# Kernel optimization log

Hardware: AMD Instinct MI355X
Metric: run time of the kernel (lower is better)

Reference implementation:

```python
import jax, jax.numpy as jnp
import numpy as np

N = 50000       # num_nodes
R = 8           # num_relations
H = 64          # hidden_channels
C = 16          # num_classes
E = 1_600_000   # num edges (avg degree 32)
T = 8192        # number of 'author' target nodes (first T nodes after to_homogeneous)


def setup_inputs() -> dict:
    key = jax.random.key(0)
    ks = jax.random.split(key, 12)
    s = 0.02
    return {
        "edge_index": jax.random.randint(ks[0], (2, E), 0, N),
        "edge_type": jax.random.randint(ks[1], (E,), 0, R),
        "num_target": T,
        # conv1 (featureless: weight is an embedding table [R, N, H], root is [N, H])
        "weight1": jax.random.normal(ks[2], (R, N, H), jnp.float32) * s,
        "root1": jax.random.normal(ks[3], (N, H), jnp.float32) * s,
        "bias1": jnp.zeros((H,), jnp.float32),
        # conv2
        "weight2": jax.random.normal(ks[4], (R, H, H), jnp.float32) * s,
        "root2": jax.random.normal(ks[5], (H, H), jnp.float32) * s,
        "bias2": jnp.zeros((H,), jnp.float32),
        # linear head
        "lin_w": jax.random.normal(ks[6], (H, C), jnp.float32) * s,
        "lin_b": jnp.zeros((C,), jnp.float32),
    }


def reference(edge_index, edge_type, num_target, weight1, root1, bias1,
              weight2, root2, bias2, lin_w, lin_b):
    src, dst = edge_index[0], edge_index[1]
    E_ = src.shape[0]

    # PyG RGCNConv aggregates with MEAN per relation, then sums over relations.
    # Count edges per (dst node, relation) to form the per-relation mean denominator.
    seg = dst * R + edge_type                          # [E] combined (node, relation) id
    cnt = jax.ops.segment_sum(jnp.ones((E_,), jnp.float32), seg, num_segments=N * R)
    scale = (1.0 / jnp.maximum(cnt, 1.0))[seg]         # [E]

    # ---- conv1: x is None -> message = weight1[edge_type][src] (embedding lookup) ----
    m1 = weight1[edge_type, src] * scale[:, None]      # [E, H]
    h1 = jax.ops.segment_sum(m1, dst, num_segments=N)  # [N, H]
    h1 = h1 + root1 + bias1                            # root1[arange(N)] == root1
    h1 = jax.nn.elu(h1)

    # ---- conv2: message = h1[src] @ weight2[edge_type] ----
    # Precompute per-relation node transforms [R, N, H], then gather per edge.
    hr = jnp.einsum('nh,rhk->rnk', h1, weight2)        # [R, N, H]
    m2 = hr[edge_type, src] * scale[:, None]           # [E, H]
    h2 = jax.ops.segment_sum(m2, dst, num_segments=N)  # [N, H]
    h2 = h2 + h1 @ root2 + bias2
    h2 = jax.nn.elu(h2)

    # ---- linear head on the target ('author') node slice ----
    out = h2[:num_target] @ lin_w + lin_b              # [T, C]
    return out
```

## Files before the change

### kernel.cpp

```cpp
#include <hip/hip_runtime.h>

#define NNODES 50000
#define NREL   8
#define HID    64
#define NCLS   16
#define NEDGE  1600000
#define NTGT   8192
#define NBINS  (NNODES * NREL)
#define CHUNK  1024
#define NCHUNK ((NBINS + CHUNK - 1) / CHUNK)

__device__ __forceinline__ float elu1(float x) { return x > 0.f ? x : expm1f(x); }

__global__ void count_kernel(const int* __restrict__ ei, const int* __restrict__ et,
                             int* __restrict__ cnt, int* __restrict__ epos) {
  int e4 = (blockIdx.x * blockDim.x + threadIdx.x) * 4;
  if (e4 >= NEDGE) return;
  int4 d = *(const int4*)(ei + NEDGE + e4);
  int4 r = *(const int4*)(et + e4);
  int4 p;
  p.x = atomicAdd(&cnt[d.x * NREL + r.x], 1);
  p.y = atomicAdd(&cnt[d.y * NREL + r.y], 1);
  p.z = atomicAdd(&cnt[d.z * NREL + r.z], 1);
  p.w = atomicAdd(&cnt[d.w * NREL + r.w], 1);
  *(int4*)(epos + e4) = p;
}

__global__ void chunk_sum_kernel(const int* __restrict__ cnt, int* __restrict__ csum) {
  __shared__ int sw[4];
  int t = threadIdx.x, lane = t & 63, wid = t >> 6;
  int i = blockIdx.x * CHUNK + t * 4;
  int s = 0;
  if (i < NBINS) { int4 c = *(const int4*)(cnt + i); s = c.x + c.y + c.z + c.w; }
#pragma unroll
  for (int off = 32; off >= 1; off >>= 1) s += __shfl_xor(s, off);
  if (lane == 0) sw[wid] = s;
  __syncthreads();
  if (t == 0) csum[blockIdx.x] = sw[0] + sw[1] + sw[2] + sw[3];
}

__global__ void scan_csum_kernel(const int* __restrict__ csum, int* __restrict__ cbase) {
  __shared__ int sw[8];
  int t = threadIdx.x, lane = t & 63, wid = t >> 6;
  int v0 = (t < NCHUNK) ? csum[t] : 0;
  int v = v0;
#pragma unroll
  for (int off = 1; off < 64; off <<= 1) {
    int u = __shfl_up(v, off);
    if (lane >= off) v += u;
  }
  if (lane == 63) sw[wid] = v;
  __syncthreads();
  if (t == 0) {
    int run = 0;
#pragma unroll
    for (int j = 0; j < 8; ++j) { int x = sw[j]; sw[j] = run; run += x; }
  }
  __syncthreads();
  if (t < NCHUNK) cbase[t] = sw[wid] + (v - v0);
}

__global__ void scan_write_kernel(const int* __restrict__ cnt, const int* __restrict__ cbase,
                                  int* __restrict__ binptr) {
  __shared__ int sw[4];
  int t = threadIdx.x, lane = t & 63, wid = t >> 6;
  int i = blockIdx.x * CHUNK + t * 4;
  int4 c = make_int4(0, 0, 0, 0);
  if (i < NBINS) c = *(const int4*)(cnt + i);
  int p0 = c.x, p1 = p0 + c.y, p2 = p1 + c.z, s = p2 + c.w;
  int v = s;
#pragma unroll
  for (int off = 1; off < 64; off <<= 1) {
    int u = __shfl_up(v, off);
    if (lane >= off) v += u;
  }
  if (lane == 63) sw[wid] = v;
  __syncthreads();
  if (t == 0) {
    int run = 0;
#pragma unroll
    for (int j = 0; j < 4; ++j) { int x = sw[j]; sw[j] = run; run += x; }
  }
  __syncthreads();
  if (i < NBINS) {
    int excl = cbase[blockIdx.x] + sw[wid] + (v - s);
    *(int4*)(binptr + i) = make_int4(excl, excl + p0, excl + p1, excl + p2);
  }
  if (blockIdx.x == 0 && t == 0) binptr[NBINS] = NEDGE;
}

__global__ void scatter_kernel(const int* __restrict__ ei, const int* __restrict__ et,
                               const int* __restrict__ epos, const int* __restrict__ binptr,
                               int2* __restrict__ epo) {
  int e4 = (blockIdx.x * blockDim.x + threadIdx.x) * 4;
  if (e4 >= NEDGE) return;
  int4 sv = *(const int4*)(ei + e4);
  int4 dv = *(const int4*)(ei + NEDGE + e4);
  int4 rv = *(const int4*)(et + e4);
  int4 pv = *(const int4*)(epos + e4);
  int srcs[4] = {sv.x, sv.y, sv.z, sv.w};
  int dsts[4] = {dv.x, dv.y, dv.z, dv.w};
  int rels[4] = {rv.x, rv.y, rv.z, rv.w};
  int poss[4] = {pv.x, pv.y, pv.z, pv.w};
#pragma unroll
  for (int j = 0; j < 4; ++j) {
    int bin = dsts[j] * NREL + rels[j];
    int b = binptr[bin];
    int c = binptr[bin + 1] - b;
    float sc = 1.0f / (float)c;
    epo[b + poss[j]] = make_int2(rels[j] * NNODES + srcs[j], __float_as_int(sc));
  }
}

__global__ __launch_bounds__(256) void conv1_kernel(
    const int* __restrict__ binptr, const int2* __restrict__ epo,
    const float* __restrict__ w1, const float* __restrict__ root1,
    const float* __restrict__ bias1, float* __restrict__ h1) {
  int wave = blockIdx.x * 4 + (threadIdx.x >> 6);
  if (wave >= NNODES) return;
  int lane = threadIdx.x & 63;
  int b0 = binptr[wave * NREL], b8 = binptr[wave * NREL + NREL];
  float acc = 0.f;
  for (int eb = b0; eb < b8; eb += 64) {
    int mb = min(64, b8 - eb);
    int2 q = epo[eb + min(lane, mb - 1)];
    int j = 0;
    for (; j + 8 <= mb; j += 8) {
      float a[8], sc[8];
#pragma unroll
      for (int u = 0; u < 8; ++u) {
        int idx = __builtin_amdgcn_readlane(q.x, j + u);
        sc[u] = __int_as_float(__builtin_amdgcn_readlane(q.y, j + u));
        a[u] = w1[(((size_t)(unsigned)idx) << 6) + lane];
      }
#pragma unroll
      for (int u = 0; u < 8; ++u) acc = fmaf(a[u], sc[u], acc);
    }
    for (; j < mb; ++j) {
      int idx = __builtin_amdgcn_readlane(q.x, j);
      float s = __int_as_float(__builtin_amdgcn_readlane(q.y, j));
      acc = fmaf(w1[(((size_t)(unsigned)idx) << 6) + lane], s, acc);
    }
  }
  float v = acc + root1[(wave << 6) + lane] + bias1[lane];
  h1[(wave << 6) + lane] = elu1(v);
}

__global__ __launch_bounds__(256) void conv2a_kernel(
    const int* __restrict__ binptr, const int2* __restrict__ epo,
    const float* __restrict__ h1, float* __restrict__ agg, int nodeBase, int nloc) {
  int wv = blockIdx.x * 4 + (threadIdx.x >> 6);
  if (wv >= nloc * NREL) return;
  int lane = threadIdx.x & 63;
  int r = wv & 7;
  int bin = (nodeBase + (wv >> 3)) * NREL + r;
  int bb = binptr[bin], ee = binptr[bin + 1];
  int rb = r * NNODES;
  float s = 0.f;
  for (int e = bb; e < ee; e += 64) {
    int mb = min(64, ee - e);
    int2 q = epo[e + min(lane, mb - 1)];
    int j = 0;
    for (; j + 4 <= mb; j += 4) {
      float a[4];
#pragma unroll
      for (int u = 0; u < 4; ++u) {
        int i0 = __builtin_amdgcn_readlane(q.x, j + u) - rb;
        a[u] = h1[(((size_t)(unsigned)i0) << 6) + lane];
      }
#pragma unroll
      for (int u = 0; u < 4; ++u) s += a[u];
    }
    for (; j < mb; ++j) {
      int i0 = __builtin_amdgcn_readlane(q.x, j) - rb;
      s += h1[(((size_t)(unsigned)i0) << 6) + lane];
    }
  }
  float out = (ee > bb) ? s * (1.0f / (float)(ee - bb)) : 0.f;
  agg[((size_t)wv << 6) + lane] = out;
}

__global__ __launch_bounds__(256, 4) void conv2b_kernel(
    const float* __restrict__ agg, const float* __restrict__ h1,
    const float* __restrict__ w2, const float* __restrict__ root2,
    const float* __restrict__ bias2, float* __restrict__ h2, int nodeBase) {
  __shared__ float sW[HID * HID];
  int t = threadIdx.x, lane = t & 63, wid = t >> 6;
  int ln0 = blockIdx.x * 8 + wid * 2;
  float bz = bias2[lane];
  float o0 = bz, o1 = bz;
  for (int r = 0; r < NREL; ++r) {
    if (r) __syncthreads();
#pragma unroll
    for (int i = 0; i < 4; ++i)
      *(float4*)(sW + t * 4 + i * 1024) = *(const float4*)(w2 + (r << 12) + t * 4 + i * 1024);
    __syncthreads();
    const float* a0 = agg + (((size_t)((ln0 + 0) * NREL + r)) << 6);
    const float* a1 = agg + (((size_t)((ln0 + 1) * NREL + r)) << 6);
#pragma unroll 16
    for (int k = 0; k < HID; ++k) {
      float w = sW[(k << 6) + lane];
      o0 = fmaf(a0[k], w, o0);
      o1 = fmaf(a1[k], w, o1);
    }
  }
  __syncthreads();
#pragma unroll
  for (int i = 0; i < 4; ++i)
    *(float4*)(sW + t * 4 + i * 1024) = *(const float4*)(root2 + t * 4 + i * 1024);
  __syncthreads();
  int g0 = nodeBase + ln0;
  const float* r0p = h1 + ((size_t)(g0 + 0) << 6);
  const float* r1p = h1 + ((size_t)(g0 + 1) << 6);
#pragma unroll 16
  for (int k = 0; k < HID; ++k) {
    float w = sW[(k << 6) + lane];
    o0 = fmaf(r0p[k], w, o0);
    o1 = fmaf(r1p[k], w, o1);
  }
  h2[((size_t)(g0 + 0) << 6) + lane] = elu1(o0);
  h2[((size_t)(g0 + 1) << 6) + lane] = elu1(o1);
}

__global__ void head_kernel(const float* __restrict__ h2, const float* __restrict__ lin_w,
                            const float* __restrict__ lin_b, float* __restrict__ out) {
  int t = blockIdx.x * blockDim.x + threadIdx.x;
  if (t >= NTGT * NCLS) return;
  int n = t >> 4, c = t & 15;
  float acc = lin_b[c];
#pragma unroll
  for (int k = 0; k < HID; ++k)
    acc = fmaf(h2[(n << 6) + k], lin_w[k * NCLS + c], acc);
  out[t] = acc;
}

extern "C" void kernel_launch(void* const* d_in, const int* in_sizes, int n_in,
                              void* d_out, int out_size, void* d_ws, size_t ws_size,
                              hipStream_t stream) {
  const int*   ei    = (const int*)d_in[0];
  const int*   et    = (const int*)d_in[1];
  const float* w1    = (const float*)d_in[3];
  const float* root1 = (const float*)d_in[4];
  const float* bias1 = (const float*)d_in[5];
  const float* w2    = (const float*)d_in[6];
  const float* root2 = (const float*)d_in[7];
  const float* bias2 = (const float*)d_in[8];
  const float* lin_w = (const float*)d_in[9];
  const float* lin_b = (const float*)d_in[10];
  float* out = (float*)d_out;

  char* ws = (char*)d_ws;
  float* h1     = (float*)ws;
  int*   cnt    = (int*)ws;
  int*   epos   = (int*)(ws + (size_t)NBINS * 4);
  char*  p      = ws + (size_t)NNODES * HID * 4;
  int*   binptr = (int*)p;  p += ((size_t)(NBINS + 1) * 4 + 255) & ~(size_t)255;
  int*   csum   = (int*)p;  p += ((size_t)NCHUNK * 4 + 255) & ~(size_t)255;
  int*   cbase  = (int*)p;  p += ((size_t)NCHUNK * 4 + 255) & ~(size_t)255;
  int2*  epo    = (int2*)p; p += (size_t)NEDGE * 8;
  float* h2     = (float*)p; p += (size_t)NTGT * HID * 4;
  float* agg    = (float*)p;
  size_t fixed  = (size_t)(p - ws);
  int chunk = (fixed + (size_t)NTGT * NREL * HID * 4 <= ws_size) ? NTGT : NTGT / 2;

  hipMemsetAsync(cnt, 0, (size_t)NBINS * sizeof(int), stream);
  count_kernel<<<(NEDGE / 4 + 255) / 256, 256, 0, stream>>>(ei, et, cnt, epos);
  chunk_sum_kernel<<<NCHUNK, 256, 0, stream>>>(cnt, csum);
  scan_csum_kernel<<<1, 512, 0, stream>>>(csum, cbase);
  scan_write_kernel<<<NCHUNK, 256, 0, stream>>>(cnt, cbase, binptr);
  scatter_kernel<<<(NEDGE / 4 + 255) / 256, 256, 0, stream>>>(ei, et, epos, binptr, epo);
  conv1_kernel<<<(NNODES + 3) / 4, 256, 0, stream>>>(binptr, epo, w1, root1, bias1, h1);
  for (int c = 0; c < NTGT / chunk; ++c) {
    conv2a_kernel<<<(chunk * NREL) / 4, 256, 0, stream>>>(binptr, epo, h1, agg, c * chunk, chunk);
    conv2b_kernel<<<chunk / 8, 256, 0, stream>>>(agg, h1, w2, root2, bias2, h2, c * chunk);
  }
  head_kernel<<<(NTGT * NCLS + 255) / 256, 256, 0, stream>>>(h2, lin_w, lin_b, out);
}
```

Before: 403.2 us.

## Gather four edges per wave with float4 row loads in conv1 and conv2a

Conv1 and conv2a previously read one float per lane per edge, with the whole wave stepping through edges one at a time using readlane. Now each wave splits into four 16-lane groups. Each group loads a full 64-float row as float4 for a different edge, and the partial sums are combined at the end with a cross-lane xor shuffle. This quadruples the memory-level parallelism per gather instruction and cuts loop iterations, at the cost of shuffles, padding masks for edge counts that are not multiples of four, and a final reduction. Only a quarter of the lanes do the final store.

```diff
diff --git a/kernel.cpp b/kernel.cpp
--- a/kernel.cpp
+++ b/kernel.cpp
@@ -119,31 +119,57 @@
   int wave = blockIdx.x * 4 + (threadIdx.x >> 6);
   if (wave >= NNODES) return;
   int lane = threadIdx.x & 63;
+  int g = lane >> 4;
+  int col = (lane & 15) << 2;
   int b0 = binptr[wave * NREL], b8 = binptr[wave * NREL + NREL];
-  float acc = 0.f;
+  float4 acc = make_float4(0.f, 0.f, 0.f, 0.f);
   for (int eb = b0; eb < b8; eb += 64) {
     int mb = min(64, b8 - eb);
     int2 q = epo[eb + min(lane, mb - 1)];
-    int j = 0;
-    for (; j + 8 <= mb; j += 8) {
-      float a[8], sc[8];
+    for (int j = 0; j < mb; j += 32) {
+      float4 a[8]; float sc[8];
 #pragma unroll
       for (int u = 0; u < 8; ++u) {
-        int idx = __builtin_amdgcn_readlane(q.x, j + u);
-        sc[u] = __int_as_float(__builtin_amdgcn_readlane(q.y, j + u));
-        a[u] = w1[(((size_t)(unsigned)idx) << 6) + lane];
+        int e0 = j + u * 4;
+        if (e0 < mb) {
+          int ei = e0 + g;
+          int eic = min(ei, mb - 1);
+          int idx = __shfl(q.x, eic);
+          float s = __int_as_float(__shfl(q.y, eic));
+          sc[u] = (ei < mb) ? s : 0.f;
+          a[u] = *(const float4*)(w1 + (((size_t)(unsigned)idx) << 6) + col);
+        } else {
+          sc[u] = 0.f;
+          a[u] = make_float4(0.f, 0.f, 0.f, 0.f);
+        }
       }
 #pragma unroll
-      for (int u = 0; u < 8; ++u) acc = fmaf(a[u], sc[u], acc);
+      for (int u = 0; u < 8; ++u) {
+        acc.x = fmaf(a[u].x, sc[u], acc.x);
+        acc.y = fmaf(a[u].y, sc[u], acc.y);
+        acc.z = fmaf(a[u].z, sc[u], acc.z);
+        acc.w = fmaf(a[u].w, sc[u], acc.w);
+      }
     }
-    for (; j < mb; ++j) {
-      int idx = __builtin_amdgcn_readlane(q.x, j);
-      float s = __int_as_float(__builtin_amdgcn_readlane(q.y, j));
-      acc = fmaf(w1[(((size_t)(unsigned)idx) << 6) + lane], s, acc);
-    }
-  }
-  float v = acc + root1[(wave << 6) + lane] + bias1[lane];
-  h1[(wave << 6) + lane] = elu1(v);
+  }
+#pragma unroll
+  for (int off = 16; off < 64; off <<= 1) {
+    acc.x += __shfl_xor(acc.x, off);
+    acc.y += __shfl_xor(acc.y, off);
+    acc.z += __shfl_xor(acc.z, off);
+    acc.w += __shfl_xor(acc.w, off);
+  }
+  if (g == 0) {
+    const float* rp = root1 + (((size_t)wave) << 6) + col;
+    float4 r = *(const float4*)rp;
+    float4 bz = *(const float4*)(bias1 + col);
+    float4 v;
+    v.x = elu1(acc.x + r.x + bz.x);
+    v.y = elu1(acc.y + r.y + bz.y);
+    v.z = elu1(acc.z + r.z + bz.z);
+    v.w = elu1(acc.w + r.w + bz.w);
+    *(float4*)(h1 + (((size_t)wave) << 6) + col) = v;
+  }
 }
 
 __global__ __launch_bounds__(256) void conv2a_kernel(
@@ -152,32 +178,53 @@
   int wv = blockIdx.x * 4 + (threadIdx.x >> 6);
   if (wv >= nloc * NREL) return;
   int lane = threadIdx.x & 63;
+  int g = lane >> 4;
+  int col = (lane & 15) << 2;
   int r = wv & 7;
   int bin = (nodeBase + (wv >> 3)) * NREL + r;
   int bb = binptr[bin], ee = binptr[bin + 1];
   int rb = r * NNODES;
-  float s = 0.f;
+  float4 s = make_float4(0.f, 0.f, 0.f, 0.f);
   for (int e = bb; e < ee; e += 64) {
     int mb = min(64, ee - e);
     int2 q = epo[e + min(lane, mb - 1)];
-    int j = 0;
-    for (; j + 4 <= mb; j += 4) {
-      float a[4];
+    for (int j = 0; j < mb; j += 16) {
+      float4 a[4]; float vld[4];
 #pragma unroll
       for (int u = 0; u < 4; ++u) {
-        int i0 = __builtin_amdgcn_readlane(q.x, j + u) - rb;
-        a[u] = h1[(((size_t)(unsigned)i0) << 6) + lane];
+        int e0 = j + u * 4;
+        if (e0 < mb) {
+          int ei = e0 + g;
+          int eic = min(ei, mb - 1);
+          int i0 = __shfl(q.x, eic) - rb;
+          vld[u] = (ei < mb) ? 1.f : 0.f;
+          a[u] = *(const float4*)(h1 + (((size_t)(unsigned)i0) << 6) + col);
+        } else {
+          vld[u] = 0.f;
+          a[u] = make_float4(0.f, 0.f, 0.f, 0.f);
+        }
       }
 #pragma unroll
-      for (int u = 0; u < 4; ++u) s += a[u];
+      for (int u = 0; u < 4; ++u) {
+        s.x = fmaf(a[u].x, vld[u], s.x);
+        s.y = fmaf(a[u].y, vld[u], s.y);
+        s.z = fmaf(a[u].z, vld[u], s.z);
+        s.w = fmaf(a[u].w, vld[u], s.w);
+      }
     }
-    for (; j < mb; ++j) {
-      int i0 = __builtin_amdgcn_readlane(q.x, j) - rb;
-      s += h1[(((size_t)(unsigned)i0) << 6) + lane];
-    }
-  }
-  float out = (ee > bb) ? s * (1.0f / (float)(ee - bb)) : 0.f;
-  agg[((size_t)wv << 6) + lane] = out;
+  }
+#pragma unroll
+  for (int off = 16; off < 64; off <<= 1) {
+    s.x += __shfl_xor(s.x, off);
+    s.y += __shfl_xor(s.y, off);
+    s.z += __shfl_xor(s.z, off);
+    s.w += __shfl_xor(s.w, off);
+  }
+  if (g == 0) {
+    float scl = (ee > bb) ? 1.0f / (float)(ee - bb) : 0.f;
+    float4 o = make_float4(s.x * scl, s.y * scl, s.z * scl, s.w * scl);
+    *(float4*)(agg + (((size_t)wv) << 6) + col) = o;
+  }
 }
 
 __global__ __launch_bounds__(256, 4) void conv2b_kernel(
```

Result: no change. 400.7 us (-0.6%).
